# Kernel tuning notes

Hardware: AMD Instinct MI355X
Metric: run time of the kernel (lower is better)

## Reference

```python
import jax, jax.numpy as jnp
import numpy as np

NEG_SLOPE = 0.2


def _gat_layer(x, W, a_src, a_dst, b, src, dst, heads, out_dim, concat):
    # x: [N, F_in]; W: [F_in, heads*out_dim]; a_src/a_dst: [heads, out_dim]
    N = x.shape[0]
    h = (x @ W).reshape(N, heads, out_dim)              # [N, H, D]
    alpha_src = jnp.sum(h * a_src[None], axis=-1)       # [N, H]
    alpha_dst = jnp.sum(h * a_dst[None], axis=-1)       # [N, H]
    e = jax.nn.leaky_relu(alpha_src[src] + alpha_dst[dst], NEG_SLOPE)  # [E, H]
    # scatter-softmax over incoming edges of each destination node
    e_max = jax.ops.segment_max(e, dst, num_segments=N)            # [N, H]
    e_exp = jnp.exp(e - e_max[dst])                                 # [E, H]
    e_sum = jax.ops.segment_sum(e_exp, dst, num_segments=N)        # [N, H]
    alpha = e_exp / e_sum[dst]                                      # [E, H]
    # weighted scatter-sum of source features
    msg = alpha[:, :, None] * h[src]                                # [E, H, D]
    out = jax.ops.segment_sum(msg, dst, num_segments=N)             # [N, H, D]
    if concat:
        out = out.reshape(N, heads * out_dim)
    else:
        out = out.mean(axis=1)
    return out + b


def setup_inputs() -> dict:
    key = jax.random.key(0)
    ks = jax.random.split(key, 9)
    N, E, F_in, C = 100000, 1600000, 512, 40
    x = jax.random.normal(ks[0], (N, F_in), dtype=jnp.float32)
    edge_index = jax.random.randint(ks[1], (2, E), 0, N, dtype=jnp.int64)
    s = 0.05
    return {
        "x": x,
        "edge_index": edge_index,
        "W1": jax.random.normal(ks[2], (F_in, 64), dtype=jnp.float32) * s,
        "att_src1": jax.random.normal(ks[3], (8, 8), dtype=jnp.float32) * s,
        "att_dst1": jax.random.normal(ks[4], (8, 8), dtype=jnp.float32) * s,
        "b1": jnp.zeros((64,), dtype=jnp.float32),
        "W2": jax.random.normal(ks[5], (64, C), dtype=jnp.float32) * s,
        "att_src2": jax.random.normal(ks[6], (1, C), dtype=jnp.float32) * s,
        "att_dst2": jax.random.normal(ks[7], (1, C), dtype=jnp.float32) * s,
        "b2": jnp.zeros((C,), dtype=jnp.float32),
    }


def reference(x, edge_index, W1, att_src1, att_dst1, b1, W2, att_src2, att_dst2, b2):
    N = x.shape[0]
    # PyG GATConv default add_self_loops=True
    loops = jnp.tile(jnp.arange(N, dtype=edge_index.dtype)[None, :], (2, 1))
    ei = jnp.concatenate([edge_index, loops], axis=1)
    src, dst = ei[0], ei[1]
    # dropout layers are identity at inference
    h = _gat_layer(x, W1, att_src1, att_dst1, b1, src, dst, heads=8, out_dim=8, concat=True)
    h = jax.nn.elu(h)
    out = _gat_layer(h, W2, att_src2, att_dst2, b2, src, dst, heads=1, out_dim=40, concat=True)
    return jax.nn.log_softmax(out, axis=1)
```

## Files before the change

### kernel.cpp

```cpp
#include <hip/hip_runtime.h>
#include <hip/hip_bf16.h>

typedef __bf16 bf16x8 __attribute__((ext_vector_type(8)));
typedef float f32x4 __attribute__((ext_vector_type(4)));
typedef unsigned u32x2 __attribute__((ext_vector_type(2)));
typedef unsigned u32x4 __attribute__((ext_vector_type(4)));

#define LR_SLOPE 0.2f
#define NBKMAX 256
#define BCAP   12288

static __device__ __forceinline__ unsigned short f2bf(float f){
  union { float f; unsigned u; } v; v.f = f;
  unsigned u = v.u;
  u += 0x7fffu + ((u >> 16) & 1u);
  return (unsigned short)(u >> 16);
}
static __device__ __forceinline__ float bf2f(unsigned short us){
  union { unsigned u; float f; } v; v.u = ((unsigned)us) << 16;
  return v.f;
}
static __device__ __forceinline__ unsigned pk2(float a, float b){
  return (unsigned)f2bf(a) | ((unsigned)f2bf(b) << 16);
}
static __device__ __forceinline__ unsigned char f2e4m3(float f){
  return (unsigned char)(__builtin_amdgcn_cvt_pk_fp8_f32(f, 0.f, 0, false) & 0xff);
}
static __device__ __forceinline__ float e4m32f(unsigned b){
  return __builtin_amdgcn_cvt_f32_fp8(b, 0);
}
typedef float f32x4v __attribute__((ext_vector_type(4)));
static __device__ __forceinline__ f32x4v ntl4(const float* p){
  return __builtin_nontemporal_load((const f32x4v*)p);
}

__global__ void prep_w_kernel(const float* __restrict__ W1, const float* __restrict__ W2,
                              unsigned short* __restrict__ wt1, unsigned short* __restrict__ wt2,
                              int* __restrict__ bcnt){
  int t = blockIdx.x*256 + threadIdx.x;
  if (t < 512*64){
    int k = t >> 6, n = t & 63;
    wt1[n*512 + k] = f2bf(W1[t]);
  } else if (t < 512*64 + 48*64){
    int t2 = t - 512*64;
    int c = t2 >> 6, k = t2 & 63;
    wt2[t2] = (c < 40) ? f2bf(W2[k*40 + c]) : (unsigned short)0;
  } else {
    int t3 = t - (512*64 + 48*64);
    if (t3 < NBKMAX) bcnt[t3] = 0;
  }
}

__global__ __launch_bounds__(256) void gemm1_kernel(
    const float* __restrict__ x, const unsigned short* __restrict__ wt1,
    const float* __restrict__ aw_s, const float* __restrict__ aw_d,
    unsigned char* __restrict__ h1p,
    unsigned short* __restrict__ as1p, float* __restrict__ ad1, int N)
{
  __shared__ unsigned short Alds[64*72];
  const int tid = threadIdx.x;
  const int wv = tid >> 6, lane = tid & 63;
  const int c0 = lane & 15, g = lane >> 4;
  const int rowbase = blockIdx.x * 64;

  const int sr = tid >> 2, sq = tid & 3;
  const int grow = rowbase + sr;
  const bool rv = grow < N;
  const float* xp = x + (size_t)grow*512 + sq*16;
  unsigned short* wls = Alds + sr*72 + sq*16;

  f32x4 acc[4];
  acc[0] = acc[1] = acc[2] = acc[3] = (f32x4){0.f,0.f,0.f,0.f};

  const unsigned short* bp0 = wt1 + (size_t)(wv*16 + c0)*512 + g*8;

  for (int kt = 0; kt < 8; ++kt){
    f32x4v f0 = {0,0,0,0}, f1 = {0,0,0,0}, f2 = {0,0,0,0}, f3 = {0,0,0,0};
    if (rv){
      const float* p = xp + kt*64;
      f0 = ntl4(p); f1 = ntl4(p+4); f2 = ntl4(p+8); f3 = ntl4(p+12);
    }
    u32x4 w0 = { pk2(f0.x,f0.y), pk2(f0.z,f0.w), pk2(f1.x,f1.y), pk2(f1.z,f1.w) };
    u32x4 w1 = { pk2(f2.x,f2.y), pk2(f2.z,f2.w), pk2(f3.x,f3.y), pk2(f3.z,f3.w) };
    if (kt) __syncthreads();
    *(u32x4*)wls       = w0;
    *(u32x4*)(wls + 8) = w1;
    __syncthreads();
    bf16x8 b0 = *(const bf16x8*)(bp0 + kt*64);
    bf16x8 b1 = *(const bf16x8*)(bp0 + kt*64 + 32);
    #pragma unroll
    for (int mi = 0; mi < 4; ++mi){
      const unsigned short* ap = Alds + (mi*16 + c0)*72 + g*8;
      bf16x8 a0 = *(const bf16x8*)ap;
      bf16x8 a1 = *(const bf16x8*)(ap + 32);
      acc[mi] = __builtin_amdgcn_mfma_f32_16x16x32_bf16(a0, b0, acc[mi], 0,0,0);
      acc[mi] = __builtin_amdgcn_mfma_f32_16x16x32_bf16(a1, b1, acc[mi], 0,0,0);
    }
  }
  const int hh = wv*2 + (c0 >> 3);
  const float aws_l = aw_s[hh*8 + (c0 & 7)];
  const float awd_l = aw_d[hh*8 + (c0 & 7)];
  #pragma unroll
  for (int mi = 0; mi < 4; ++mi){
    #pragma unroll
    for (int i = 0; i < 4; ++i){
      int row = rowbase + mi*16 + 4*g + i;
      float av = acc[mi][i];
      if (row < N) h1p[(size_t)row*64 + wv*16 + c0] = f2e4m3(av);
      float ss = av * aws_l;
      float dd = av * awd_l;
      ss += __shfl_xor(ss, 1); ss += __shfl_xor(ss, 2); ss += __shfl_xor(ss, 4);
      dd += __shfl_xor(dd, 1); dd += __shfl_xor(dd, 2); dd += __shfl_xor(dd, 4);
      if (row < N && (c0 & 7) == 0){
        as1p[row*8 + hh] = f2bf(ss);
        ad1[row*8 + hh]  = dd;
      }
    }
  }
}

__global__ __launch_bounds__(256) void bucketA_kernel(
    const int* __restrict__ ei, int* __restrict__ bcnt,
    unsigned* __restrict__ bucketed, int E, int M, int NBK)
{
  __shared__ int hist[NBKMAX];
  __shared__ int gb[NBKMAX];
  const int tid = threadIdx.x;
  const int t0 = blockIdx.x * 2048;
  for (int i = tid; i < NBK; i += 256) hist[i] = 0;
  __syncthreads();

  unsigned pe[8]; int bk[8], rnk[8];
  #pragma unroll
  for (int j = 0; j < 8; ++j){
    int m = t0 + j*256 + tid;
    if (m < M){
      int s, d;
      if (m < E){ s = ei[m]; d = ei[E + m]; }
      else      { s = d = m - E; }
      bk[j] = d >> 9;
      pe[j] = ((unsigned)s << 9) | (unsigned)(d & 511);
      rnk[j] = atomicAdd(&hist[bk[j]], 1);
    } else bk[j] = -1;
  }
  __syncthreads();
  for (int i = tid; i < NBK; i += 256) gb[i] = atomicAdd(&bcnt[i], hist[i]);
  __syncthreads();
  #pragma unroll
  for (int j = 0; j < 8; ++j){
    if (bk[j] >= 0) bucketed[(size_t)bk[j]*BCAP + gb[bk[j]] + rnk[j]] = pe[j];
  }
}

__global__ __launch_bounds__(512) void bucketB_kernel(
    const unsigned* __restrict__ bucketed, const int* __restrict__ bcnt,
    int* __restrict__ rowstart, int* __restrict__ csr, int N, int M, int NBK)
{
  __shared__ int cnt[512];
  __shared__ int cur[512];
  __shared__ int basevar;
  const int k = blockIdx.x;
  const int nodebase = k << 9;
  const int nn = min(512, N - nodebase);
  const int t = threadIdx.x;

  cur[t] = (t < NBK) ? bcnt[t] : 0;
  __syncthreads();
  for (int off = 1; off < 256; off <<= 1){
    int u = (t >= off && t < 256) ? cur[t-off] : 0;
    __syncthreads();
    if (t < 256) cur[t] += u;
    __syncthreads();
  }
  if (t == 0) basevar = (k > 0) ? cur[k-1] : 0;
  cnt[t] = 0;
  __syncthreads();

  const int ck = bcnt[k];
  const unsigned* bp = bucketed + (size_t)k*BCAP;
  for (int m = t; m < ck; m += 512) atomicAdd(&cnt[bp[m] & 511], 1);
  __syncthreads();
  int myc = cnt[t];
  cur[t] = myc; __syncthreads();
  for (int off = 1; off < 512; off <<= 1){
    int u = (t >= off) ? cur[t-off] : 0;
    __syncthreads();
    cur[t] += u;
    __syncthreads();
  }
  const int base = basevar;
  int excl = base + cur[t] - myc;
  if (t < nn) rowstart[nodebase + t] = excl;
  if (k == 0 && t == 0) rowstart[N] = M;
  cnt[t] = excl;
  __syncthreads();
  for (int m = t; m < ck; m += 512){
    unsigned e = bp[m];
    int pos = atomicAdd(&cnt[e & 511], 1);
    csr[pos] = (int)(e >> 9);
  }
}

__global__ __launch_bounds__(256) void l1agg_kernel(
    const int* __restrict__ rowstart, const int* __restrict__ csr,
    const unsigned short* __restrict__ as1p,
    const float* __restrict__ ad1,
    const unsigned char* __restrict__ h1p,
    const float* __restrict__ b1,
    unsigned short* __restrict__ g1b, int N)
{
  int wid = blockIdx.x*4 + (threadIdx.x >> 6);
  if (wid >= N) return;
  const int lane = threadIdx.x & 63;
  const int jq  = lane >> 3;
  const int hq  = lane & 7;
  const int par = lane >> 4;
  const int q   = lane & 15;
  const int hh  = q >> 1;
  int r0 = rowstart[wid], r1 = rowstart[wid+1];
  int cnt = r1 - r0;
  int cap = cnt < 64 ? cnt : 64;
  int myidx = csr[r0 + (lane < cap ? lane : cap-1)];
  const float advq = ad1[wid*8 + hq];

  float a0 = 0.f, a1 = 0.f, a2 = 0.f, a3 = 0.f, den = 0.f;
  for (int c = 0; c < cap; c += 8){
    int se = __shfl(myidx, c + jq);
    float t = bf2f(as1p[se*8 + hq]) + advq;
    t = (t > 0.f) ? t : LR_SLOPE*t;
    float w = __expf(t);
    if (c + jq >= cap) w = 0.f;
    den += w;
    #pragma unroll
    for (int j = 0; j < 2; ++j){
      int s8 = 4*j + par;
      int sj = __shfl(myidx, c + s8);
      float wj = __shfl(w, s8*8 + hh);
      unsigned hv = *(const unsigned*)(h1p + (size_t)sj*64 + 4*q);
      a0 = fmaf(wj, __builtin_amdgcn_cvt_f32_fp8(hv, 0), a0);
      a1 = fmaf(wj, __builtin_amdgcn_cvt_f32_fp8(hv, 1), a1);
      a2 = fmaf(wj, __builtin_amdgcn_cvt_f32_fp8(hv, 2), a2);
      a3 = fmaf(wj, __builtin_amdgcn_cvt_f32_fp8(hv, 3), a3);
    }
  }
  for (int r = r0 + 64; r < r1; ++r){
    int sx = csr[r];
    float t = bf2f(as1p[sx*8 + hq]) + advq;
    t = (t > 0.f) ? t : LR_SLOPE*t;
    float w = __expf(t);
    if (lane < 8) den += w;
    float wj = __shfl(w, hh);
    if (par == 0){
      unsigned hv = *(const unsigned*)(h1p + (size_t)sx*64 + 4*q);
      a0 = fmaf(wj, __builtin_amdgcn_cvt_f32_fp8(hv, 0), a0);
      a1 = fmaf(wj, __builtin_amdgcn_cvt_f32_fp8(hv, 1), a1);
      a2 = fmaf(wj, __builtin_amdgcn_cvt_f32_fp8(hv, 2), a2);
      a3 = fmaf(wj, __builtin_amdgcn_cvt_f32_fp8(hv, 3), a3);
    }
  }
  den += __shfl_xor(den, 8); den += __shfl_xor(den, 16); den += __shfl_xor(den, 32);
  a0 += __shfl_xor(a0, 16); a0 += __shfl_xor(a0, 32);
  a1 += __shfl_xor(a1, 16); a1 += __shfl_xor(a1, 32);
  a2 += __shfl_xor(a2, 16); a2 += __shfl_xor(a2, 32);
  a3 += __shfl_xor(a3, 16); a3 += __shfl_xor(a3, 32);
  if (lane < 16){
    float rdv = 1.f / __shfl(den, hh);
    float v0 = fmaf(a0, rdv, b1[4*q]);
    float v1 = fmaf(a1, rdv, b1[4*q + 1]);
    float v2 = fmaf(a2, rdv, b1[4*q + 2]);
    float v3 = fmaf(a3, rdv, b1[4*q + 3]);
    v0 = (v0 > 0.f) ? v0 : (__expf(v0) - 1.f);
    v1 = (v1 > 0.f) ? v1 : (__expf(v1) - 1.f);
    v2 = (v2 > 0.f) ? v2 : (__expf(v2) - 1.f);
    v3 = (v3 > 0.f) ? v3 : (__expf(v3) - 1.f);
    u32x2 pk = { pk2(v0, v1), pk2(v2, v3) };
    *(u32x2*)(g1b + (size_t)wid*64 + 4*q) = pk;
  }
}

__global__ __launch_bounds__(256) void gemm2_kernel(
    const unsigned short* __restrict__ g1b, const unsigned short* __restrict__ wt2,
    const float* __restrict__ aw_s, const float* __restrict__ aw_d,
    unsigned char* __restrict__ h2x, float* __restrict__ ad2, int N)
{
  __shared__ unsigned short Alds[64*72];
  const int tid = threadIdx.x;
  const int wv = tid >> 6, lane = tid & 63;
  const int c0 = lane & 15, g = lane >> 4;
  const int rowbase = blockIdx.x * 64;

  const int sr = tid >> 2, sq = tid & 3;
  const int grow = rowbase + sr;
  const bool rv = grow < N;
  u32x4 w0 = {0,0,0,0}, w1 = {0,0,0,0};
  if (rv){
    const u32x4* gp = (const u32x4*)(g1b + (size_t)grow*64 + sq*16);
    w0 = gp[0];
    w1 = gp[1];
  }
  unsigned short* wls = Alds + sr*72 + sq*16;
  *(u32x4*)wls       = w0;
  *(u32x4*)(wls + 8) = w1;
  __syncthreads();

  f32x4 acc[3];
  acc[0] = acc[1] = acc[2] = (f32x4){0.f,0.f,0.f,0.f};
  #pragma unroll
  for (int t2 = 0; t2 < 2; ++t2){
    const unsigned short* ap = Alds + (wv*16 + c0)*72 + t2*32 + g*8;
    bf16x8 a = *(const bf16x8*)ap;
    #pragma unroll
    for (int nf = 0; nf < 3; ++nf){
      bf16x8 b = *(const bf16x8*)(wt2 + (nf*16 + c0)*64 + t2*32 + g*8);
      acc[nf] = __builtin_amdgcn_mfma_f32_16x16x32_bf16(a, b, acc[nf], 0,0,0);
    }
  }
  float aws[3], awd[3];
  aws[0] = aw_s[c0];      awd[0] = aw_d[c0];
  aws[1] = aw_s[16 + c0]; awd[1] = aw_d[16 + c0];
  aws[2] = (c0 < 8) ? aw_s[32 + c0] : 0.f;
  awd[2] = (c0 < 8) ? aw_d[32 + c0] : 0.f;
  #pragma unroll
  for (int i = 0; i < 4; ++i){
    int row = rowbase + wv*16 + 4*g + i;
    float ss = 0.f, dd = 0.f;
    #pragma unroll
    for (int nf = 0; nf < 3; ++nf){
      int col = nf*16 + c0;
      float av = acc[nf][i];
      if (row < N && col < 40) h2x[(size_t)row*64 + 4 + col] = f2e4m3(av);
      float m = (col < 40) ? av : 0.f;
      ss = fmaf(m, aws[nf], ss);
      dd = fmaf(m, awd[nf], dd);
    }
    ss += __shfl_xor(ss, 1); ss += __shfl_xor(ss, 2);
    ss += __shfl_xor(ss, 4); ss += __shfl_xor(ss, 8);
    dd += __shfl_xor(dd, 1); dd += __shfl_xor(dd, 2);
    dd += __shfl_xor(dd, 4); dd += __shfl_xor(dd, 8);
    if (row < N && c0 == 0){
      *(float*)(h2x + (size_t)row*64) = ss;
      ad2[row] = dd;
    }
  }
}

__global__ __launch_bounds__(256) void l2agg_kernel(
    const int* __restrict__ rowstart, const int* __restrict__ csr,
    const unsigned char* __restrict__ h2x, const float* __restrict__ ad2,
    const float* __restrict__ b2, float* __restrict__ out, int N)
{
  int wid = blockIdx.x*4 + (threadIdx.x >> 6);
  if (wid >= N) return;
  const int lane = threadIdx.x & 63;
  const int eg = lane / 11;
  const int il = lane - eg*11;
  const bool valid = eg < 5;
  int r0 = rowstart[wid], r1 = rowstart[wid+1];
  int cnt = r1 - r0;
  int cap = cnt < 64 ? cnt : 64;
  int myidx = csr[r0 + (lane < cap ? lane : cap-1)];
  const float adv = ad2[wid];

  float a0 = 0.f, a1 = 0.f, a2 = 0.f, a3 = 0.f, den = 0.f;
  for (int c = 0; c < cap; c += 5){
    int slot = c + eg;
    int slc  = slot < cap ? slot : cap-1;
    int sj = __shfl(myidx, slc);
    unsigned hv = valid ? *(const unsigned*)(h2x + (size_t)sj*64 + 4*il) : 0u;
    union { unsigned u; float f; } cv; cv.u = hv;
    float t = cv.f + adv;
    t = (t > 0.f) ? t : LR_SLOPE*t;
    float w = __expf(t);
    if (slot >= cap || !valid) w = 0.f;
    if (il == 0) den += w;
    float wj = __shfl(w, eg*11);
    a0 = fmaf(wj, __builtin_amdgcn_cvt_f32_fp8(hv, 0), a0);
    a1 = fmaf(wj, __builtin_amdgcn_cvt_f32_fp8(hv, 1), a1);
    a2 = fmaf(wj, __builtin_amdgcn_cvt_f32_fp8(hv, 2), a2);
    a3 = fmaf(wj, __builtin_amdgcn_cvt_f32_fp8(hv, 3), a3);
  }
  for (int r = r0 + 64; r < r1; ++r){
    int sx = csr[r];
    unsigned hv = valid ? *(const unsigned*)(h2x + (size_t)sx*64 + 4*il) : 0u;
    union { unsigned u; float f; } cv; cv.u = hv;
    float t = cv.f + adv;
    t = (t > 0.f) ? t : LR_SLOPE*t;
    float w = __expf(t);
    float wj = __shfl(w, 0);
    if (lane == 0) den += wj;
    if (eg == 0){
      a0 = fmaf(wj, __builtin_amdgcn_cvt_f32_fp8(hv, 0), a0);
      a1 = fmaf(wj, __builtin_amdgcn_cvt_f32_fp8(hv, 1), a1);
      a2 = fmaf(wj, __builtin_amdgcn_cvt_f32_fp8(hv, 2), a2);
      a3 = fmaf(wj, __builtin_amdgcn_cvt_f32_fp8(hv, 3), a3);
    }
  }
  #pragma unroll
  for (int off = 32; off; off >>= 1) den += __shfl_xor(den, off);
  float t0 = a0, t1 = a1, t2 = a2, t3 = a3;
  #pragma unroll
  for (int gix = 1; gix < 5; ++gix){
    int src = ((eg + gix) % 5)*11 + il;
    t0 += __shfl(a0, src);
    t1 += __shfl(a1, src);
    t2 += __shfl(a2, src);
    t3 += __shfl(a3, src);
  }
  const bool outl = (eg == 0) && (il >= 1);
  const int fb = (il - 1)*4;
  float rdv = 1.f/den;
  float v0 = outl ? fmaf(t0, rdv, b2[fb])     : -1e30f;
  float v1 = outl ? fmaf(t1, rdv, b2[fb + 1]) : -1e30f;
  float v2 = outl ? fmaf(t2, rdv, b2[fb + 2]) : -1e30f;
  float v3 = outl ? fmaf(t3, rdv, b2[fb + 3]) : -1e30f;
  float m = fmaxf(fmaxf(v0, v1), fmaxf(v2, v3));
  #pragma unroll
  for (int off = 32; off; off >>= 1) m = fmaxf(m, __shfl_xor(m, off));
  float sum = outl ? (__expf(v0-m) + __expf(v1-m) + __expf(v2-m) + __expf(v3-m)) : 0.f;
  #pragma unroll
  for (int off = 32; off; off >>= 1) sum += __shfl_xor(sum, off);
  if (outl){
    float ls = m + __logf(sum);
    f32x4 o = { v0 - ls, v1 - ls, v2 - ls, v3 - ls };
    *(f32x4*)(out + (size_t)wid*40 + fb) = o;
  }
}

extern "C" void kernel_launch(void* const* d_in, const int* in_sizes, int n_in,
                              void* d_out, int out_size, void* d_ws, size_t ws_size,
                              hipStream_t stream)
{
  const float* x   = (const float*)d_in[0];
  const int*   ei  = (const int*)d_in[1];
  const float* W1  = (const float*)d_in[2];
  const float* aS1 = (const float*)d_in[3];
  const float* aD1 = (const float*)d_in[4];
  const float* b1  = (const float*)d_in[5];
  const float* W2  = (const float*)d_in[6];
  const float* aS2 = (const float*)d_in[7];
  const float* aD2 = (const float*)d_in[8];
  const float* b2  = (const float*)d_in[9];

  const int N   = in_sizes[0] / 512;
  const int E   = in_sizes[1] / 2;
  const int M   = E + N;
  const int NBK = (N + 511) >> 9;

  char* base = (char*)d_ws;
  size_t off = 0;
  auto alloc = [&](size_t bytes)->char* {
    char* p = base + off;
    off += (bytes + 255) & ~(size_t)255;
    return p;
  };
  unsigned char*  h1p  = (unsigned char*)alloc((size_t)N*64);
  unsigned short* g1b  = (unsigned short*)alloc((size_t)N*64*2);
  unsigned short* as1p = (unsigned short*)alloc((size_t)N*8*2);
  float* ad1      = (float*)alloc((size_t)N*8*4);
  int*   rowstart = (int*)alloc((size_t)(N+1)*4);
  int*   bcnt     = (int*)alloc((size_t)NBKMAX*4);
  int*   csr      = (int*)alloc((size_t)M*4);
  unsigned* bucketed = (unsigned*)alloc((size_t)NBKMAX*BCAP*4);
  unsigned short* wt1 = (unsigned short*)alloc(64*512*2);
  unsigned short* wt2 = (unsigned short*)alloc(48*64*2);
  unsigned char* h2x = h1p;
  float* ad2 = (float*)ad1;
  float* outp = (float*)d_out;

  prep_w_kernel<<<141, 256, 0, stream>>>(W1, W2, wt1, wt2, bcnt);
  gemm1_kernel<<<(N+63)/64, 256, 0, stream>>>(x, wt1, aS1, aD1, h1p, as1p, ad1, N);
  bucketA_kernel<<<(M+2047)/2048, 256, 0, stream>>>(ei, bcnt, bucketed, E, M, NBK);
  bucketB_kernel<<<NBK, 512, 0, stream>>>(bucketed, bcnt, rowstart, csr, N, M, NBK);
  l1agg_kernel<<<(N+3)/4, 256, 0, stream>>>(rowstart, csr, as1p, ad1, h1p, b1, g1b, N);
  gemm2_kernel<<<(N+63)/64, 256, 0, stream>>>(g1b, wt2, aS2, aD2, h2x, ad2, N);
  l2agg_kernel<<<(N+3)/4, 256, 0, stream>>>(rowstart, csr, h2x, ad2, b2, outp, N);
}
```

Measured before the change: 253.4 us.

## Fuse layer-2 linear transform into layer-1 aggregation kernel

Removes the separate gemm2 kernel and the bf16 g1 intermediate buffer. Each wave now keeps its node's 64 ELU outputs in shared memory and computes the 40 layer-2 features with scalar FMAs against a shared-memory copy of W2, then writes the fp8 h2x row, the source attention score and ad2 directly. This saves a kernel launch and an N×64 bf16 round trip through global memory. In exchange, every 4-node block reloads and repacks W2 into LDS, and the MFMA matmul is replaced by per-lane scalar math. h2x and ad2 get their own buffers because they can no longer alias inputs that are still being read.

After: 282.6 us. 11.5% more time.

```diff
diff --git a/kernel.cpp b/kernel.cpp
--- a/kernel.cpp
+++ b/kernel.cpp
@@ -207,11 +207,25 @@
     const float* __restrict__ ad1,
     const unsigned char* __restrict__ h1p,
     const float* __restrict__ b1,
-    unsigned short* __restrict__ g1b, int N)
-{
-  int wid = blockIdx.x*4 + (threadIdx.x >> 6);
+    const unsigned short* __restrict__ wt2,
+    const float* __restrict__ aw_s2, const float* __restrict__ aw_d2,
+    unsigned char* __restrict__ h2x, float* __restrict__ ad2, int N)
+{
+  __shared__ unsigned w2l[32*40];
+  __shared__ float g1buf[4][64];
+  const int tid = threadIdx.x;
+  for (int idx = tid; idx < 40*32; idx += 256){
+    int c = idx >> 5, k2 = idx & 31;
+    unsigned lo = wt2[c*64 + 2*k2];
+    unsigned hi = wt2[c*64 + 2*k2 + 1];
+    w2l[k2*40 + c] = lo | (hi << 16);
+  }
+  __syncthreads();
+
+  const int wvid = tid >> 6;
+  int wid = blockIdx.x*4 + wvid;
   if (wid >= N) return;
-  const int lane = threadIdx.x & 63;
+  const int lane = tid & 63;
   const int jq  = lane >> 3;
   const int hq  = lane & 7;
   const int par = lane >> 4;
@@ -273,75 +287,30 @@
     v1 = (v1 > 0.f) ? v1 : (__expf(v1) - 1.f);
     v2 = (v2 > 0.f) ? v2 : (__expf(v2) - 1.f);
     v3 = (v3 > 0.f) ? v3 : (__expf(v3) - 1.f);
-    u32x2 pk = { pk2(v0, v1), pk2(v2, v3) };
-    *(u32x2*)(g1b + (size_t)wid*64 + 4*q) = pk;
-  }
-}
-
-__global__ __launch_bounds__(256) void gemm2_kernel(
-    const unsigned short* __restrict__ g1b, const unsigned short* __restrict__ wt2,
-    const float* __restrict__ aw_s, const float* __restrict__ aw_d,
-    unsigned char* __restrict__ h2x, float* __restrict__ ad2, int N)
-{
-  __shared__ unsigned short Alds[64*72];
-  const int tid = threadIdx.x;
-  const int wv = tid >> 6, lane = tid & 63;
-  const int c0 = lane & 15, g = lane >> 4;
-  const int rowbase = blockIdx.x * 64;
-
-  const int sr = tid >> 2, sq = tid & 3;
-  const int grow = rowbase + sr;
-  const bool rv = grow < N;
-  u32x4 w0 = {0,0,0,0}, w1 = {0,0,0,0};
-  if (rv){
-    const u32x4* gp = (const u32x4*)(g1b + (size_t)grow*64 + sq*16);
-    w0 = gp[0];
-    w1 = gp[1];
-  }
-  unsigned short* wls = Alds + sr*72 + sq*16;
-  *(u32x4*)wls       = w0;
-  *(u32x4*)(wls + 8) = w1;
-  __syncthreads();
-
-  f32x4 acc[3];
-  acc[0] = acc[1] = acc[2] = (f32x4){0.f,0.f,0.f,0.f};
-  #pragma unroll
-  for (int t2 = 0; t2 < 2; ++t2){
-    const unsigned short* ap = Alds + (wv*16 + c0)*72 + t2*32 + g*8;
-    bf16x8 a = *(const bf16x8*)ap;
-    #pragma unroll
-    for (int nf = 0; nf < 3; ++nf){
-      bf16x8 b = *(const bf16x8*)(wt2 + (nf*16 + c0)*64 + t2*32 + g*8);
-      acc[nf] = __builtin_amdgcn_mfma_f32_16x16x32_bf16(a, b, acc[nf], 0,0,0);
-    }
-  }
-  float aws[3], awd[3];
-  aws[0] = aw_s[c0];      awd[0] = aw_d[c0];
-  aws[1] = aw_s[16 + c0]; awd[1] = aw_d[16 + c0];
-  aws[2] = (c0 < 8) ? aw_s[32 + c0] : 0.f;
-  awd[2] = (c0 < 8) ? aw_d[32 + c0] : 0.f;
-  #pragma unroll
-  for (int i = 0; i < 4; ++i){
-    int row = rowbase + wv*16 + 4*g + i;
-    float ss = 0.f, dd = 0.f;
-    #pragma unroll
-    for (int nf = 0; nf < 3; ++nf){
-      int col = nf*16 + c0;
-      float av = acc[nf][i];
-      if (row < N && col < 40) h2x[(size_t)row*64 + 4 + col] = f2e4m3(av);
-      float m = (col < 40) ? av : 0.f;
-      ss = fmaf(m, aws[nf], ss);
-      dd = fmaf(m, awd[nf], dd);
-    }
-    ss += __shfl_xor(ss, 1); ss += __shfl_xor(ss, 2);
-    ss += __shfl_xor(ss, 4); ss += __shfl_xor(ss, 8);
-    dd += __shfl_xor(dd, 1); dd += __shfl_xor(dd, 2);
-    dd += __shfl_xor(dd, 4); dd += __shfl_xor(dd, 8);
-    if (row < N && c0 == 0){
-      *(float*)(h2x + (size_t)row*64) = ss;
-      ad2[row] = dd;
-    }
-  }
+    *(f32x4*)&g1buf[wvid][4*q] = (f32x4){v0, v1, v2, v3};
+  }
+  __asm__ volatile("s_waitcnt lgkmcnt(0)" ::: "memory");
+
+  const int cc = (lane < 40) ? lane : 0;
+  const float* gb = g1buf[wvid];
+  float hc = 0.f;
+  #pragma unroll
+  for (int k2 = 0; k2 < 32; ++k2){
+    float ga = gb[2*k2];
+    float gbv = gb[2*k2 + 1];
+    unsigned wp = w2l[k2*40 + cc];
+    hc = fmaf(ga,  bf2f((unsigned short)(wp & 0xffff)),
+         fmaf(gbv, bf2f((unsigned short)(wp >> 16)), hc));
+  }
+  float ss = (lane < 40) ? hc * aw_s2[cc] : 0.f;
+  float dd = (lane < 40) ? hc * aw_d2[cc] : 0.f;
+  #pragma unroll
+  for (int off = 32; off; off >>= 1){ ss += __shfl_xor(ss, off); dd += __shfl_xor(dd, off); }
+  if (lane == 0){
+    *(float*)(h2x + (size_t)wid*64) = ss;
+    ad2[wid] = dd;
+  }
+  if (lane < 40) h2x[(size_t)wid*64 + 4 + lane] = f2e4m3(hc);
 }
 
 __global__ __launch_bounds__(256) void l2agg_kernel(
@@ -454,24 +423,23 @@
     return p;
   };
   unsigned char*  h1p  = (unsigned char*)alloc((size_t)N*64);
-  unsigned short* g1b  = (unsigned short*)alloc((size_t)N*64*2);
+  unsigned char*  h2x  = (unsigned char*)alloc((size_t)N*64);
   unsigned short* as1p = (unsigned short*)alloc((size_t)N*8*2);
   float* ad1      = (float*)alloc((size_t)N*8*4);
+  float* ad2      = (float*)alloc((size_t)N*4);
   int*   rowstart = (int*)alloc((size_t)(N+1)*4);
   int*   bcnt     = (int*)alloc((size_t)NBKMAX*4);
   int*   csr      = (int*)alloc((size_t)M*4);
   unsigned* bucketed = (unsigned*)alloc((size_t)NBKMAX*BCAP*4);
   unsigned short* wt1 = (unsigned short*)alloc(64*512*2);
   unsigned short* wt2 = (unsigned short*)alloc(48*64*2);
-  unsigned char* h2x = h1p;
-  float* ad2 = (float*)ad1;
   float* outp = (float*)d_out;
 
   prep_w_kernel<<<141, 256, 0, stream>>>(W1, W2, wt1, wt2, bcnt);
   gemm1_kernel<<<(N+63)/64, 256, 0, stream>>>(x, wt1, aS1, aD1, h1p, as1p, ad1, N);
   bucketA_kernel<<<(M+2047)/2048, 256, 0, stream>>>(ei, bcnt, bucketed, E, M, NBK);
   bucketB_kernel<<<NBK, 512, 0, stream>>>(bucketed, bcnt, rowstart, csr, N, M, NBK);
-  l1agg_kernel<<<(N+3)/4, 256, 0, stream>>>(rowstart, csr, as1p, ad1, h1p, b1, g1b, N);
-  gemm2_kernel<<<(N+63)/64, 256, 0, stream>>>(g1b, wt2, aS2, aD2, h2x, ad2, N);
+  l1agg_kernel<<<(N+3)/4, 256, 0, stream>>>(rowstart, csr, as1p, ad1, h1p, b1,
+                                            wt2, aS2, aD2, h2x, ad2, N);
   l2agg_kernel<<<(N+3)/4, 256, 0, stream>>>(rowstart, csr, h2x, ad2, b2, outp, N);
 }
```
